# Kernel optimization log

Hardware: AMD Instinct MI355X
Metric: run time of the kernel (lower is better)

The kernel has to match this reference:

```python
import jax, jax.numpy as jnp
import numpy as np

B, C, H, W = 8, 128, 64, 64
GROUPS = 8
EPS = 1e-5


def setup_inputs() -> dict:
    key = jax.random.key(0)
    ks = jax.random.split(key, 4)
    x = jax.random.normal(ks[0], (B, C, H, W), dtype=jnp.float32)
    gamma = jnp.ones((C,), jnp.float32)
    beta = jnp.zeros((C,), jnp.float32)
    w_qkv = jax.random.normal(ks[1], (3 * C, C), jnp.float32) * (C ** -0.5)
    b_qkv = jnp.zeros((3 * C,), jnp.float32)
    w_proj = jax.random.normal(ks[2], (C, C), jnp.float32) * (C ** -0.5)
    b_proj = jnp.zeros((C,), jnp.float32)
    return {"x": x, "gamma": gamma, "beta": beta, "w_qkv": w_qkv,
            "b_qkv": b_qkv, "w_proj": w_proj, "b_proj": b_proj}


def group_norm(x, gamma, beta):
    b, c, h, w = x.shape
    xg = x.reshape(b, GROUPS, c // GROUPS, h, w)
    mean = xg.mean(axis=(2, 3, 4), keepdims=True)
    var = xg.var(axis=(2, 3, 4), keepdims=True)
    xn = ((xg - mean) * jax.lax.rsqrt(var + EPS)).reshape(b, c, h, w)
    return xn * gamma[None, :, None, None] + beta[None, :, None, None]


def reference(x, gamma, beta, w_qkv, b_qkv, w_proj, b_proj):
    b, c, h, w = x.shape
    n = h * w
    hn = group_norm(x, gamma, beta)
    # 1x1 conv == channel matmul
    qkv = jnp.einsum('oc,bchw->bohw', w_qkv, hn) + b_qkv[None, :, None, None]
    q, k, v = jnp.split(qkv.reshape(b, 3 * c, n), 3, axis=1)  # each [b,c,n]
    attn = jax.nn.softmax(jnp.einsum('bci,bcj->bij', q, k) * (c ** -0.5), axis=-1)
    out = jnp.einsum('bij,bcj->bci', attn, v).reshape(b, c, h, w)
    proj = jnp.einsum('oc,bchw->bohw', w_proj, out) + b_proj[None, :, None, None]
    return x + proj
```

## Files before the change

### kernel.cpp

```cpp
#include <hip/hip_runtime.h>
#include <cstdint>

#define NB 8
#define NC 128
#define NPIX 4096
#define NGROUP 8
#define CPG 16
#define EPS_GN 1e-5f
#define QSCALE 0.12751879523604132f
#define NSPLIT 2
#define JTILES (NPIX / 64 / NSPLIT)

typedef __attribute__((ext_vector_type(8))) short short8;
typedef __attribute__((ext_vector_type(16))) float f32x16;

typedef __attribute__((address_space(1))) const void gvoid_t;
typedef __attribute__((address_space(3))) void svoid_t;

__device__ __forceinline__ unsigned packbf(float lo, float hi) {
  unsigned r;
  asm("v_cvt_pk_bf16_f32 %0, %1, %2" : "=v"(r) : "v"(lo), "v"(hi));
  return r;
}

__device__ __forceinline__ int swK(int row) {
  return ((row & 7) << 1) | ((row >> 3) & 1);
}

__global__ __launch_bounds__(256) void k_gn_stats(const float* __restrict__ x,
                                                  float* __restrict__ stats) {
  int blk = blockIdx.x;
  const float4* base = (const float4*)(x + (size_t)blk * CPG * NPIX);
  float s = 0.f, ss = 0.f;
  for (int i = threadIdx.x; i < CPG * NPIX / 4; i += 256) {
    float4 v = base[i];
    s  += v.x + v.y + v.z + v.w;
    ss += v.x * v.x + v.y * v.y + v.z * v.z + v.w * v.w;
  }
#pragma unroll
  for (int off = 32; off >= 1; off >>= 1) {
    s  += __shfl_down(s, off);
    ss += __shfl_down(ss, off);
  }
  __shared__ float red[8];
  int wid = threadIdx.x >> 6;
  if ((threadIdx.x & 63) == 0) { red[wid] = s; red[4 + wid] = ss; }
  __syncthreads();
  if (threadIdx.x == 0) {
    float S  = red[0] + red[1] + red[2] + red[3];
    float SS = red[4] + red[5] + red[6] + red[7];
    float mean = S * (1.f / (CPG * NPIX));
    float var  = SS * (1.f / (CPG * NPIX)) - mean * mean;
    stats[blk * 2]     = mean;
    stats[blk * 2 + 1] = rsqrtf(var + EPS_GN);
  }
}

__global__ __launch_bounds__(256) void k_qkv(const float* __restrict__ x,
                                             const float* __restrict__ stats,
                                             const float* __restrict__ gamma,
                                             const float* __restrict__ beta,
                                             const float* __restrict__ w,
                                             const float* __restrict__ bias,
                                             ushort* __restrict__ qT,
                                             ushort* __restrict__ kT,
                                             ushort* __restrict__ vB) {
  __shared__ ushort At[128 * 128];
  __shared__ ushort Bt[128 * 128];
  __shared__ float sArr[128], tArr[128], biasS[384];
  int b = blockIdx.x, pt = blockIdx.y;
  int p0 = pt * 128;
  int tid = threadIdx.x;
  if (tid < 128) {
    int g = tid >> 4;
    float mean = stats[(b * NGROUP + g) * 2];
    float rstd = stats[(b * NGROUP + g) * 2 + 1];
    float sc = rstd * gamma[tid];
    sArr[tid] = sc;
    tArr[tid] = beta[tid] - mean * sc;
  }
  for (int i = tid; i < 384; i += 256) biasS[i] = bias[i];
  __syncthreads();
  const float* xb = x + (size_t)b * NC * NPIX;
#pragma unroll
  for (int u = 0; u < 8; ++u) {
    int task = tid + u * 256;
    int p = task & 127, cc = task >> 7;
    int c0 = cc * 8;
    float v[8];
#pragma unroll
    for (int i = 0; i < 8; ++i)
      v[i] = sArr[c0 + i] * xb[(size_t)(c0 + i) * NPIX + p0 + p] + tArr[c0 + i];
    uint4 pk;
    pk.x = packbf(v[0], v[1]); pk.y = packbf(v[2], v[3]);
    pk.z = packbf(v[4], v[5]); pk.w = packbf(v[6], v[7]);
    *(uint4*)&Bt[((p << 4) + (cc ^ (p & 7))) << 3] = pk;
  }
  int lane = tid & 63, wv = tid >> 6;
  int lq = lane & 31, h = lane >> 5;

  for (int ot = 0; ot < 3; ++ot) {
    __syncthreads();
#pragma unroll
    for (int u = 0; u < 8; ++u) {
      int task = tid + u * 256;
      int o = task >> 4, cc = task & 15;
      const float* wp = w + ((size_t)(ot * 128 + o)) * 128 + cc * 8;
      float4 a = *(const float4*)wp;
      float4 bq = *(const float4*)(wp + 4);
      uint4 pk;
      pk.x = packbf(a.x, a.y);  pk.y = packbf(a.z, a.w);
      pk.z = packbf(bq.x, bq.y); pk.w = packbf(bq.z, bq.w);
      *(uint4*)&At[((o << 4) + (cc ^ (o & 7))) << 3] = pk;
    }
    __syncthreads();
    short8 af[8];
    int arow = wv * 32 + lq;
#pragma unroll
    for (int kk = 0; kk < 8; ++kk) {
      int ch = kk * 2 + h;
      af[kk] = *(const short8*)&At[((arow << 4) + (ch ^ (arow & 7))) << 3];
    }
#pragma unroll
    for (int np = 0; np < 2; ++np) {
      int nt0 = np * 2, nt1 = np * 2 + 1;
      int br0 = nt0 * 32 + lq, br1 = nt1 * 32 + lq;
      f32x16 a0, a1;
#pragma unroll
      for (int r = 0; r < 16; ++r) { a0[r] = 0.f; a1[r] = 0.f; }
      __builtin_amdgcn_s_setprio(1);
#pragma unroll
      for (int kk = 0; kk < 8; ++kk) {
        int ch = kk * 2 + h;
        short8 h0 = *(const short8*)&Bt[((br0 << 4) + (ch ^ (br0 & 7))) << 3];
        short8 h1 = *(const short8*)&Bt[((br1 << 4) + (ch ^ (br1 & 7))) << 3];
        a0 = __builtin_amdgcn_mfma_f32_32x32x16_bf16(af[kk], h0, a0, 0, 0, 0);
        a1 = __builtin_amdgcn_mfma_f32_32x32x16_bf16(af[kk], h1, a1, 0, 0, 0);
      }
      __builtin_amdgcn_s_setprio(0);
#pragma unroll
      for (int half = 0; half < 2; ++half) {
        f32x16& acc = half ? a1 : a0;
        int pg = p0 + (half ? nt1 : nt0) * 32 + lq;
        if (ot < 2) {
          ushort* dst = (ot == 0) ? qT : kT;
          float sc = (ot == 0) ? QSCALE : 1.0f;
#pragma unroll
          for (int g2 = 0; g2 < 4; ++g2) {
            int orow = wv * 32 + 4 * h + 8 * g2;
            uint2 st;
            st.x = packbf((acc[g2 * 4 + 0] + biasS[ot * 128 + orow + 0]) * sc,
                          (acc[g2 * 4 + 1] + biasS[ot * 128 + orow + 1]) * sc);
            st.y = packbf((acc[g2 * 4 + 2] + biasS[ot * 128 + orow + 2]) * sc,
                          (acc[g2 * 4 + 3] + biasS[ot * 128 + orow + 3]) * sc);
            *(uint2*)&dst[(((size_t)b << 12) + pg) * 128 + orow] = st;
          }
        } else {
#pragma unroll
          for (int r = 0; r < 16; ++r) {
            int orow = wv * 32 + (r & 3) + 8 * (r >> 2) + 4 * h;
            float vv = acc[r] + biasS[256 + orow];
            vB[((size_t)(b * 128 + orow) << 12) + pg] = (ushort)(packbf(vv, vv) & 0xffffu);
          }
        }
      }
    }
  }
}

__device__ __forceinline__ void attn_tile(const ushort* __restrict__ cur,
                                          const short8 (&qf)[8],
                                          f32x16 (&pacc)[4],
                                          float& m_run, float& l_run,
                                          int lq, int h, int swk) {
  f32x16 s0, s1;
#pragma unroll
  for (int r = 0; r < 16; ++r) { s0[r] = 0.f; s1[r] = 0.f; }
  __builtin_amdgcn_s_setprio(1);
#pragma unroll
  for (int kk = 0; kk < 8; ++kk) {
    int ch = (kk << 1) + h;
    short8 kf0 = *(const short8*)&cur[(((lq) << 4) + (ch ^ swk)) << 3];
    short8 kf1 = *(const short8*)&cur[(((32 + lq) << 4) + (ch ^ swk)) << 3];
    s0 = __builtin_amdgcn_mfma_f32_32x32x16_bf16(kf0, qf[kk], s0, 0, 0, 0);
    s1 = __builtin_amdgcn_mfma_f32_32x32x16_bf16(kf1, qf[kk], s1, 0, 0, 0);
  }
  __builtin_amdgcn_s_setprio(0);

  float tm[8];
#pragma unroll
  for (int r = 0; r < 8; ++r)
    tm[r] = fmaxf(fmaxf(s0[2 * r], s0[2 * r + 1]), fmaxf(s1[2 * r], s1[2 * r + 1]));
  float tmax = fmaxf(fmaxf(fmaxf(tm[0], tm[1]), fmaxf(tm[2], tm[3])),
                     fmaxf(fmaxf(tm[4], tm[5]), fmaxf(tm[6], tm[7])));
  tmax = fmaxf(tmax, __shfl_xor(tmax, 32));

  bool noresc = __all(tmax - m_run <= 8.f);
  float mcur = noresc ? m_run : fmaxf(m_run, tmax);

#pragma unroll
  for (int r = 0; r < 16; ++r) { s0[r] = exp2f(s0[r] - mcur); }
#pragma unroll
  for (int r = 0; r < 16; ++r) { s1[r] = exp2f(s1[r] - mcur); }
  float a0 = (s0[0] + s0[1]) + (s0[2] + s0[3]);
  float a1 = (s0[4] + s0[5]) + (s0[6] + s0[7]);
  float a2 = (s0[8] + s0[9]) + (s0[10] + s0[11]);
  float a3 = (s0[12] + s0[13]) + (s0[14] + s0[15]);
  float a4 = (s1[0] + s1[1]) + (s1[2] + s1[3]);
  float a5 = (s1[4] + s1[5]) + (s1[6] + s1[7]);
  float a6 = (s1[8] + s1[9]) + (s1[10] + s1[11]);
  float a7 = (s1[12] + s1[13]) + (s1[14] + s1[15]);
  float sum = ((a0 + a1) + (a2 + a3)) + ((a4 + a5) + (a6 + a7));
  sum += __shfl_xor(sum, 32);

  if (noresc) {
    l_run += sum;
  } else {
    float alpha = exp2f(m_run - mcur);
    m_run = mcur;
    l_run = l_run * alpha + sum;
#pragma unroll
    for (int r = 0; r < 16; ++r) {
      int qr = (r & 3) + ((r >> 2) << 3) + (h << 2);
      float av = __shfl(alpha, qr);
      pacc[0][r] *= av; pacc[1][r] *= av; pacc[2][r] *= av; pacc[3][r] *= av;
    }
  }

  short8 pa[4];
#pragma unroll
  for (int kk = 0; kk < 4; ++kk) {
    float v0, v1, v2, v3, v4, v5, v6, v7;
    if (kk == 0)      { v0=s0[0];v1=s0[1];v2=s0[2];v3=s0[3];v4=s0[4];v5=s0[5];v6=s0[6];v7=s0[7]; }
    else if (kk == 1) { v0=s0[8];v1=s0[9];v2=s0[10];v3=s0[11];v4=s0[12];v5=s0[13];v6=s0[14];v7=s0[15]; }
    else if (kk == 2) { v0=s1[0];v1=s1[1];v2=s1[2];v3=s1[3];v4=s1[4];v5=s1[5];v6=s1[6];v7=s1[7]; }
    else              { v0=s1[8];v1=s1[9];v2=s1[10];v3=s1[11];v4=s1[12];v5=s1[13];v6=s1[14];v7=s1[15]; }
    unsigned P0a = packbf(v0, v1), P0b = packbf(v2, v3);
    unsigned P1a = packbf(v4, v5), P1b = packbf(v6, v7);
    unsigned sA = h ? P0a : P1a, sB = h ? P0b : P1b;
    unsigned rA = (unsigned)__shfl_xor((int)sA, 32);
    unsigned rB = (unsigned)__shfl_xor((int)sB, 32);
    uint4 wv;
    wv.x = h ? rA : P0a;  wv.y = h ? rB : P0b;
    wv.z = h ? P1a : rA;  wv.w = h ? P1b : rB;
    pa[kk] = __builtin_bit_cast(short8, wv);
  }

  __builtin_amdgcn_s_setprio(1);
#pragma unroll
  for (int nt = 0; nt < 4; ++nt) {
    int row = (nt << 5) + lq;
#pragma unroll
    for (int kk = 0; kk < 4; ++kk) {
      int ch = (kk << 1) + h;
      short8 vf = *(const short8*)&cur[8192 + (((row << 3) + (ch ^ (lq & 7))) << 3)];
      pacc[nt] = __builtin_amdgcn_mfma_f32_32x32x16_bf16(pa[kk], vf, pacc[nt], 0, 0, 0);
    }
  }
  __builtin_amdgcn_s_setprio(0);
}

__global__ __launch_bounds__(256, 2) void k_attn(const ushort* __restrict__ qT,
                                                 const ushort* __restrict__ kT,
                                                 const ushort* __restrict__ vB,
                                                 float* __restrict__ attP,
                                                 float2* __restrict__ mlv) {
  __shared__ ushort lds[32768];
  int tid = threadIdx.x;
  int b = blockIdx.x, qt = blockIdx.y, s = blockIdx.z;
  int wid = tid >> 6;
  int lane = tid & 63;
  int lq = lane & 31;
  int h = lane >> 5;
  int swk = swK(lq);
  int q0 = qt * 128 + wid * 32;
  int jbase = s * (NPIX / NSPLIT);

  short8 qf[8];
  const ushort* qp = qT + (((size_t)b << 12) + q0 + lq) * 128 + h * 8;
#pragma unroll
  for (int kk = 0; kk < 8; ++kk) qf[kk] = *(const short8*)(qp + kk * 16);

  f32x16 pacc[4];
#pragma unroll
  for (int nt = 0; nt < 4; ++nt)
#pragma unroll
    for (int r = 0; r < 16; ++r) pacc[nt][r] = 0.f;
  float m_run = -1e30f, l_run = 0.f;

  int id0 = wid * 64 + lane;
  int krow0 = id0 >> 4, kch0 = id0 & 15;
  int vrow0 = id0 >> 3, vch0 = id0 & 7;
  const ushort* kbase = kT + (((size_t)b << 12) + jbase + krow0) * 128 +
                        ((kch0 ^ swK(krow0)) << 3);
  const ushort* vbase = vB + ((size_t)(b * 128 + vrow0) << 12) + jbase +
                        ((vch0 ^ (vrow0 & 7)) << 3);
  int tstage = 0;

#define STAGE(SEL)                                                              \
  do {                                                                          \
    if (tstage < JTILES) {                                                      \
      ushort* dbase = lds + (SEL) * 16384;                                      \
      _Pragma("unroll") for (int u = 0; u < 4; ++u) {                           \
        __builtin_amdgcn_global_load_lds((gvoid_t*)(kbase + u * 2048),          \
            (svoid_t*)(dbase + (u * 4 + wid) * 512), 16, 0, 0);                 \
        __builtin_amdgcn_global_load_lds((gvoid_t*)(vbase + u * 131072),        \
            (svoid_t*)(dbase + 8192 + (u * 4 + wid) * 512), 16, 0, 0);          \
      }                                                                         \
      kbase += 8192;                                       \
      vbase += 64;                                                 \
      ++tstage;                                                                 \
    }                                                                           \
  } while (0)

  STAGE(0);
  for (int it = 0; it < JTILES / 2; ++it) {
    __syncthreads();
    STAGE(1);
    attn_tile(lds, qf, pacc, m_run, l_run, lq, h, swk);
    __syncthreads();
    STAGE(0);
    attn_tile(lds + 16384, qf, pacc, m_run, l_run, lq, h, swk);
  }
#undef STAGE

  size_t sb = (size_t)(s * NB + b);
#pragma unroll
  for (int r = 0; r < 16; ++r) {
    int qr = (r & 3) + ((r >> 2) << 3) + (h << 2);
    size_t rowbase = (((sb << 12) + q0 + qr) << 7) + lq;
    attP[rowbase]      = pacc[0][r];
    attP[rowbase + 32] = pacc[1][r];
    attP[rowbase + 64] = pacc[2][r];
    attP[rowbase + 96] = pacc[3][r];
  }
  if (h == 0) {
    mlv[(sb << 12) + q0 + lq] = make_float2(m_run, l_run);
  }
}

__global__ __launch_bounds__(256) void k_proj(const float* __restrict__ x,
                                              const float* __restrict__ attP,
                                              const float2* __restrict__ mlv,
                                              const float* __restrict__ w,
                                              const float* __restrict__ bias,
                                              float* __restrict__ out) {
  __shared__ ushort At[128 * 128];
  __shared__ ushort Bt[128 * 128];
  __shared__ float c0s[128], c1s[128], biasS[128];
  int b = blockIdx.x, pt = blockIdx.y;
  int p0 = pt * 128;
  int tid = threadIdx.x;
  if (tid < 128) {
    float2 ml0 = mlv[(((size_t)b) << 12) + p0 + tid];
    float2 ml1 = mlv[(((size_t)(NB + b)) << 12) + p0 + tid];
    float M = fmaxf(ml0.x, ml1.x);
    float e0 = exp2f(ml0.x - M), e1 = exp2f(ml1.x - M);
    float inv = 1.f / (ml0.y * e0 + ml1.y * e1);
    c0s[tid] = e0 * inv;
    c1s[tid] = e1 * inv;
    biasS[tid] = bias[tid];
  }
  __syncthreads();
#pragma unroll
  for (int u = 0; u < 8; ++u) {
    int task = tid + u * 256;
    int p = task & 127, cc = task >> 7;
    const float* a0 = attP + ((((size_t)b << 12) + p0 + p) << 7) + cc * 8;
    const float* a1 = attP + ((((size_t)(NB + b) << 12) + p0 + p) << 7) + cc * 8;
    float c0 = c0s[p], c1 = c1s[p];
    float v[8];
    float4 x0 = *(const float4*)a0, x0b = *(const float4*)(a0 + 4);
    float4 x1 = *(const float4*)a1, x1b = *(const float4*)(a1 + 4);
    v[0] = x0.x * c0 + x1.x * c1;  v[1] = x0.y * c0 + x1.y * c1;
    v[2] = x0.z * c0 + x1.z * c1;  v[3] = x0.w * c0 + x1.w * c1;
    v[4] = x0b.x * c0 + x1b.x * c1; v[5] = x0b.y * c0 + x1b.y * c1;
    v[6] = x0b.z * c0 + x1b.z * c1; v[7] = x0b.w * c0 + x1b.w * c1;
    uint4 pk;
    pk.x = packbf(v[0], v[1]); pk.y = packbf(v[2], v[3]);
    pk.z = packbf(v[4], v[5]); pk.w = packbf(v[6], v[7]);
    *(uint4*)&Bt[((p << 4) + (cc ^ (p & 7))) << 3] = pk;
  }
#pragma unroll
  for (int u = 0; u < 8; ++u) {
    int task = tid + u * 256;
    int o = task >> 4, cc = task & 15;
    const float* wp = w + (size_t)o * 128 + cc * 8;
    float4 a = *(const float4*)wp;
    float4 bq = *(const float4*)(wp + 4);
    uint4 pk;
    pk.x = packbf(a.x, a.y);  pk.y = packbf(a.z, a.w);
    pk.z = packbf(bq.x, bq.y); pk.w = packbf(bq.z, bq.w);
    *(uint4*)&At[((o << 4) + (cc ^ (o & 7))) << 3] = pk;
  }
  __syncthreads();
  int lane = tid & 63, wv = tid >> 6;
  int lq = lane & 31, h = lane >> 5;
  short8 af[8];
  int arow = wv * 32 + lq;
#pragma unroll
  for (int kk = 0; kk < 8; ++kk) {
    int ch = kk * 2 + h;
    af[kk] = *(const short8*)&At[((arow << 4) + (ch ^ (arow & 7))) << 3];
  }
  const float* xb = x + (size_t)b * NC * NPIX;
  float* ob = out + (size_t)b * NC * NPIX;
#pragma unroll
  for (int np = 0; np < 2; ++np) {
    int nt0 = np * 2, nt1 = np * 2 + 1;
    int br0 = nt0 * 32 + lq, br1 = nt1 * 32 + lq;
    f32x16 a0, a1;
#pragma unroll
    for (int r = 0; r < 16; ++r) { a0[r] = 0.f; a1[r] = 0.f; }
    __builtin_amdgcn_s_setprio(1);
#pragma unroll
    for (int kk = 0; kk < 8; ++kk) {
      int ch = kk * 2 + h;
      short8 h0 = *(const short8*)&Bt[((br0 << 4) + (ch ^ (br0 & 7))) << 3];
      short8 h1 = *(const short8*)&Bt[((br1 << 4) + (ch ^ (br1 & 7))) << 3];
      a0 = __builtin_amdgcn_mfma_f32_32x32x16_bf16(af[kk], h0, a0, 0, 0, 0);
      a1 = __builtin_amdgcn_mfma_f32_32x32x16_bf16(af[kk], h1, a1, 0, 0, 0);
    }
    __builtin_amdgcn_s_setprio(0);
#pragma unroll
    for (int half = 0; half < 2; ++half) {
      f32x16& acc = half ? a1 : a0;
      int pg = p0 + (half ? nt1 : nt0) * 32 + lq;
#pragma unroll
      for (int r = 0; r < 16; ++r) {
        int orow = wv * 32 + (r & 3) + 8 * (r >> 2) + 4 * h;
        size_t idx = ((size_t)orow << 12) + pg;
        ob[idx] = acc[r] + biasS[orow] + xb[idx];
      }
    }
  }
}

extern "C" void kernel_launch(void* const* d_in, const int* in_sizes, int n_in,
                              void* d_out, int out_size, void* d_ws, size_t ws_size,
                              hipStream_t stream) {
  const float* x      = (const float*)d_in[0];
  const float* gamma  = (const float*)d_in[1];
  const float* beta   = (const float*)d_in[2];
  const float* w_qkv  = (const float*)d_in[3];
  const float* b_qkv  = (const float*)d_in[4];
  const float* w_proj = (const float*)d_in[5];
  const float* b_proj = (const float*)d_in[6];
  float* out = (float*)d_out;
  char* wsb = (char*)d_ws;

  float*  stats  = (float*)wsb;
  ushort* qT     = (ushort*)(wsb + 1024);
  ushort* kT     = (ushort*)(wsb + 1024 + (8u << 20));
  ushort* vB     = (ushort*)(wsb + 1024 + (16u << 20));
  float*  attP   = (float*)(wsb + 1024 + (24u << 20));
  float2* mlv    = (float2*)(wsb + 1024 + (56u << 20));

  hipLaunchKernelGGL(k_gn_stats, dim3(NB * NGROUP), dim3(256), 0, stream, x, stats);
  hipLaunchKernelGGL(k_qkv, dim3(NB, NPIX / 128), dim3(256), 0, stream,
                     x, stats, gamma, beta, w_qkv, b_qkv, qT, kT, vB);
  hipLaunchKernelGGL(k_attn, dim3(NB, NPIX / 128, NSPLIT), dim3(256), 0, stream,
                     qT, kT, vB, attP, mlv);
  hipLaunchKernelGGL(k_proj, dim3(NB, NPIX / 128), dim3(256), 0, stream,
                     x, attP, mlv, w_proj, b_proj, out);
}
```

Baseline: 144.0 us.

## Store attention partials in bf16 and pre-convert weights with direct LDS loads

Adds a small kernel that converts the QKV and projection weights once into a pre-swizzled bf16 buffer. The qkv and proj kernels then fill shared memory from it with global_load_lds instead of converting fp32 per block. The split-attention partial outputs are written as bf16 rather than fp32, which halves the intermediate write and read traffic between the attention and projection kernels. The trade-offs are an extra kernel launch and slightly lower precision on the partial accumulators before they are combined.

```diff
diff --git a/kernel.cpp b/kernel.cpp
--- a/kernel.cpp
+++ b/kernel.cpp
@@ -22,9 +22,34 @@
   asm("v_cvt_pk_bf16_f32 %0, %1, %2" : "=v"(r) : "v"(lo), "v"(hi));
   return r;
 }
+__device__ __forceinline__ ushort bf16of(float v) {
+  return (ushort)(packbf(v, v) & 0xffffu);
+}
+__device__ __forceinline__ float bfl(unsigned w) {
+  return __builtin_bit_cast(float, w << 16);
+}
+__device__ __forceinline__ float bfh(unsigned w) {
+  return __builtin_bit_cast(float, w & 0xffff0000u);
+}
 
 __device__ __forceinline__ int swK(int row) {
   return ((row & 7) << 1) | ((row >> 3) & 1);
+}
+
+__global__ __launch_bounds__(256) void k_wprep(const float* __restrict__ wqkv,
+                                               const float* __restrict__ wproj,
+                                               ushort* __restrict__ wbuf) {
+  int gi = blockIdx.x * 256 + threadIdx.x;
+  int t = gi >> 11, ci = gi & 2047;
+  int o = ci >> 4, cc = (ci & 15) ^ (o & 7);
+  const float* src = (t < 3) ? (wqkv + ((size_t)(t * 128 + o) * 128 + cc * 8))
+                             : (wproj + ((size_t)o * 128 + cc * 8));
+  float4 a = *(const float4*)src;
+  float4 b2 = *(const float4*)(src + 4);
+  uint4 pk;
+  pk.x = packbf(a.x, a.y);  pk.y = packbf(a.z, a.w);
+  pk.z = packbf(b2.x, b2.y); pk.w = packbf(b2.z, b2.w);
+  *(uint4*)&wbuf[(size_t)gi << 3] = pk;
 }
 
 __global__ __launch_bounds__(256) void k_gn_stats(const float* __restrict__ x,
@@ -60,7 +85,7 @@
                                              const float* __restrict__ stats,
                                              const float* __restrict__ gamma,
                                              const float* __restrict__ beta,
-                                             const float* __restrict__ w,
+                                             const ushort* __restrict__ wbuf,
                                              const float* __restrict__ bias,
                                              ushort* __restrict__ qT,
                                              ushort* __restrict__ kT,
@@ -103,15 +128,10 @@
     __syncthreads();
 #pragma unroll
     for (int u = 0; u < 8; ++u) {
-      int task = tid + u * 256;
-      int o = task >> 4, cc = task & 15;
-      const float* wp = w + ((size_t)(ot * 128 + o)) * 128 + cc * 8;
-      float4 a = *(const float4*)wp;
-      float4 bq = *(const float4*)(wp + 4);
-      uint4 pk;
-      pk.x = packbf(a.x, a.y);  pk.y = packbf(a.z, a.w);
-      pk.z = packbf(bq.x, bq.y); pk.w = packbf(bq.z, bq.w);
-      *(uint4*)&At[((o << 4) + (cc ^ (o & 7))) << 3] = pk;
+      int g = u * 4 + wv;
+      __builtin_amdgcn_global_load_lds(
+          (gvoid_t*)(wbuf + (((size_t)ot * 2048 + g * 64 + lane) << 3)),
+          (svoid_t*)(At + (g << 9)), 16, 0, 0);
     }
     __syncthreads();
     short8 af[8];
@@ -160,7 +180,7 @@
           for (int r = 0; r < 16; ++r) {
             int orow = wv * 32 + (r & 3) + 8 * (r >> 2) + 4 * h;
             float vv = acc[r] + biasS[256 + orow];
-            vB[((size_t)(b * 128 + orow) << 12) + pg] = (ushort)(packbf(vv, vv) & 0xffffu);
+            vB[((size_t)(b * 128 + orow) << 12) + pg] = bf16of(vv);
           }
         }
       }
@@ -263,7 +283,7 @@
 __global__ __launch_bounds__(256, 2) void k_attn(const ushort* __restrict__ qT,
                                                  const ushort* __restrict__ kT,
                                                  const ushort* __restrict__ vB,
-                                                 float* __restrict__ attP,
+                                                 ushort* __restrict__ attP,
                                                  float2* __restrict__ mlv) {
   __shared__ ushort lds[32768];
   int tid = threadIdx.x;
@@ -329,10 +349,10 @@
   for (int r = 0; r < 16; ++r) {
     int qr = (r & 3) + ((r >> 2) << 3) + (h << 2);
     size_t rowbase = (((sb << 12) + q0 + qr) << 7) + lq;
-    attP[rowbase]      = pacc[0][r];
-    attP[rowbase + 32] = pacc[1][r];
-    attP[rowbase + 64] = pacc[2][r];
-    attP[rowbase + 96] = pacc[3][r];
+    attP[rowbase]      = bf16of(pacc[0][r]);
+    attP[rowbase + 32] = bf16of(pacc[1][r]);
+    attP[rowbase + 64] = bf16of(pacc[2][r]);
+    attP[rowbase + 96] = bf16of(pacc[3][r]);
   }
   if (h == 0) {
     mlv[(sb << 12) + q0 + lq] = make_float2(m_run, l_run);
@@ -340,9 +360,9 @@
 }
 
 __global__ __launch_bounds__(256) void k_proj(const float* __restrict__ x,
-                                              const float* __restrict__ attP,
+                                              const ushort* __restrict__ attP,
                                               const float2* __restrict__ mlv,
-                                              const float* __restrict__ w,
+                                              const ushort* __restrict__ wbuf,
                                               const float* __restrict__ bias,
                                               float* __restrict__ out) {
   __shared__ ushort At[128 * 128];
@@ -351,6 +371,14 @@
   int b = blockIdx.x, pt = blockIdx.y;
   int p0 = pt * 128;
   int tid = threadIdx.x;
+  int lane = tid & 63, wv = tid >> 6;
+#pragma unroll
+  for (int u = 0; u < 8; ++u) {
+    int g = u * 4 + wv;
+    __builtin_amdgcn_global_load_lds(
+        (gvoid_t*)(wbuf + (((size_t)3 * 2048 + g * 64 + lane) << 3)),
+        (svoid_t*)(At + (g << 9)), 16, 0, 0);
+  }
   if (tid < 128) {
     float2 ml0 = mlv[(((size_t)b) << 12) + p0 + tid];
     float2 ml1 = mlv[(((size_t)(NB + b)) << 12) + p0 + tid];
@@ -366,35 +394,23 @@
   for (int u = 0; u < 8; ++u) {
     int task = tid + u * 256;
     int p = task & 127, cc = task >> 7;
-    const float* a0 = attP + ((((size_t)b << 12) + p0 + p) << 7) + cc * 8;
-    const float* a1 = attP + ((((size_t)(NB + b) << 12) + p0 + p) << 7) + cc * 8;
+    const ushort* a0p = attP + ((((size_t)b << 12) + p0 + p) << 7) + cc * 8;
+    const ushort* a1p = attP + ((((size_t)(NB + b) << 12) + p0 + p) << 7) + cc * 8;
+    uint4 u0 = *(const uint4*)a0p;
+    uint4 u1 = *(const uint4*)a1p;
     float c0 = c0s[p], c1 = c1s[p];
-    float v[8];
-    float4 x0 = *(const float4*)a0, x0b = *(const float4*)(a0 + 4);
-    float4 x1 = *(const float4*)a1, x1b = *(const float4*)(a1 + 4);
-    v[0] = x0.x * c0 + x1.x * c1;  v[1] = x0.y * c0 + x1.y * c1;
-    v[2] = x0.z * c0 + x1.z * c1;  v[3] = x0.w * c0 + x1.w * c1;
-    v[4] = x0b.x * c0 + x1b.x * c1; v[5] = x0b.y * c0 + x1b.y * c1;
-    v[6] = x0b.z * c0 + x1b.z * c1; v[7] = x0b.w * c0 + x1b.w * c1;
     uint4 pk;
-    pk.x = packbf(v[0], v[1]); pk.y = packbf(v[2], v[3]);
-    pk.z = packbf(v[4], v[5]); pk.w = packbf(v[6], v[7]);
+    pk.x = packbf(bfl(u0.x) * c0 + bfl(u1.x) * c1,
+                  bfh(u0.x) * c0 + bfh(u1.x) * c1);
+    pk.y = packbf(bfl(u0.y) * c0 + bfl(u1.y) * c1,
+                  bfh(u0.y) * c0 + bfh(u1.y) * c1);
+    pk.z = packbf(bfl(u0.z) * c0 + bfl(u1.z) * c1,
+                  bfh(u0.z) * c0 + bfh(u1.z) * c1);
+    pk.w = packbf(bfl(u0.w) * c0 + bfl(u1.w) * c1,
+                  bfh(u0.w) * c0 + bfh(u1.w) * c1);
     *(uint4*)&Bt[((p << 4) + (cc ^ (p & 7))) << 3] = pk;
   }
-#pragma unroll
-  for (int u = 0; u < 8; ++u) {
-    int task = tid + u * 256;
-    int o = task >> 4, cc = task & 15;
-    const float* wp = w + (size_t)o * 128 + cc * 8;
-    float4 a = *(const float4*)wp;
-    float4 bq = *(const float4*)(wp + 4);
-    uint4 pk;
-    pk.x = packbf(a.x, a.y);  pk.y = packbf(a.z, a.w);
-    pk.z = packbf(bq.x, bq.y); pk.w = packbf(bq.z, bq.w);
-    *(uint4*)&At[((o << 4) + (cc ^ (o & 7))) << 3] = pk;
-  }
   __syncthreads();
-  int lane = tid & 63, wv = tid >> 6;
   int lq = lane & 31, h = lane >> 5;
   short8 af[8];
   int arow = wv * 32 + lq;
@@ -449,18 +465,20 @@
   float* out = (float*)d_out;
   char* wsb = (char*)d_ws;
 
-  float*  stats  = (float*)wsb;
-  ushort* qT     = (ushort*)(wsb + 1024);
-  ushort* kT     = (ushort*)(wsb + 1024 + (8u << 20));
-  ushort* vB     = (ushort*)(wsb + 1024 + (16u << 20));
-  float*  attP   = (float*)(wsb + 1024 + (24u << 20));
-  float2* mlv    = (float2*)(wsb + 1024 + (56u << 20));
-
+  float*  stats = (float*)wsb;
+  ushort* qT    = (ushort*)(wsb + 1024);
+  ushort* kT    = (ushort*)(wsb + 1024 + (8u << 20));
+  ushort* vB    = (ushort*)(wsb + 1024 + (16u << 20));
+  ushort* attP  = (ushort*)(wsb + 1024 + (24u << 20));
+  float2* mlv   = (float2*)(wsb + 1024 + (40u << 20));
+  ushort* wbuf  = (ushort*)(wsb + 1024 + (41u << 20));
+
+  hipLaunchKernelGGL(k_wprep, dim3(32), dim3(256), 0, stream, w_qkv, w_proj, wbuf);
   hipLaunchKernelGGL(k_gn_stats, dim3(NB * NGROUP), dim3(256), 0, stream, x, stats);
   hipLaunchKernelGGL(k_qkv, dim3(NB, NPIX / 128), dim3(256), 0, stream,
-                     x, stats, gamma, beta, w_qkv, b_qkv, qT, kT, vB);
+                     x, stats, gamma, beta, wbuf, b_qkv, qT, kT, vB);
   hipLaunchKernelGGL(k_attn, dim3(NB, NPIX / 128, NSPLIT), dim3(256), 0, stream,
                      qT, kT, vB, attP, mlv);
   hipLaunchKernelGGL(k_proj, dim3(NB, NPIX / 128), dim3(256), 0, stream,
-                     x, attP, mlv, w_proj, b_proj, out);
-}
+                     x, attP, mlv, wbuf, b_proj, out);
+}
```

Result: no change. 144.3 us (+0.2%).
